# Optimization experiments

Hardware: AMD Instinct MI355X
Metric: run time of the kernel (lower is better)

## Reference

```python
import jax, jax.numpy as jnp
import numpy as np

M, K, N = 8192, 4096, 4096


def setup_inputs() -> dict:
    key = jax.random.key(0)
    k1, k2, k3 = jax.random.split(key, 3)
    inp = jax.random.normal(k1, (M, K), dtype=jnp.float32)
    weight = jax.random.normal(k2, (N, K), dtype=jnp.float32)
    bias = jax.random.normal(k3, (N,), dtype=jnp.bfloat16)
    return {"inp": inp, "weight": weight, "bias": bias}


def reference(inp, weight, bias):
    # FP8TensorMeta scales are all ones in the source module.
    scale = jnp.float32(1.0)       # quantization scale
    scale_inv = jnp.float32(1.0)   # dequantization scale (per operand)

    # cast_to_fp8: scale then saturate-cast to e4m3
    inp_fp8 = (inp * scale).astype(jnp.float8_e4m3fn)
    weight_fp8 = (weight * scale).astype(jnp.float8_e4m3fn)

    # fp8_gemm: dequantized GEMM with fp32 accumulation, bf16 bias, fp32 out
    out = jnp.einsum(
        "mk,nk->mn",
        inp_fp8.astype(jnp.float32),
        weight_fp8.astype(jnp.float32),
    ) * (scale_inv * scale_inv)
    out = out + bias.astype(jnp.float32)[None, :]
    return out
```

## Files before the change

kernel.cpp:

```cpp
#include <hip/hip_runtime.h>
#include <hip/hip_bf16.h>
#include <stdint.h>


#define MD 8192
#define KD 4096
#define ND 4096
#define BM 128
#define BN 128
#define BK 64

using f32x4  = __attribute__((ext_vector_type(4))) float;
using f32x16 = __attribute__((ext_vector_type(16))) float;
using i32x4  = __attribute__((ext_vector_type(4))) int;
using i32x8  = __attribute__((ext_vector_type(8))) int;

__global__ __launch_bounds__(256) void quant_fp8_fused_kernel(
    const float* __restrict__ inA, const float* __restrict__ inW,
    uint8_t* __restrict__ outA, uint8_t* __restrict__ outW) {
  const int NA4 = MD * KD / 4;
  const int NW4 = ND * KD / 4;
  const int tid = blockIdx.x * blockDim.x + threadIdx.x;
  const int stride = gridDim.x * blockDim.x;

  for (int i = tid; i < NA4; i += stride) {
    float4 f = ((const float4*)inA)[i];
    int v = 0;
    v = __builtin_amdgcn_cvt_pk_fp8_f32(f.x, f.y, v, false);
    v = __builtin_amdgcn_cvt_pk_fp8_f32(f.z, f.w, v, true);
    ((int*)outA)[i] = v;
  }
  for (int i = tid; i < NW4; i += stride) {
    float4 f = ((const float4*)inW)[i];
    int v = 0;
    v = __builtin_amdgcn_cvt_pk_fp8_f32(f.x, f.y, v, false);
    v = __builtin_amdgcn_cvt_pk_fp8_f32(f.z, f.w, v, true);
    ((int*)outW)[i] = v;
  }
}

__device__ __forceinline__ void gload16(const uint8_t* g, uint8_t* l) {
  __builtin_amdgcn_global_load_lds(
      (const __attribute__((address_space(1))) void*)g,
      (__attribute__((address_space(3))) void*)l, 16, 0, 0);
}

__global__ __launch_bounds__(256, 2) void fp8mx_gemm_bias_kernel(
    const uint8_t* __restrict__ A, const uint8_t* __restrict__ B,
    const __hip_bfloat16* __restrict__ bias, float* __restrict__ C) {
  __shared__ uint8_t sm[2][2][BM * BK];

  const int bid = blockIdx.x;
  const int chunk = bid & 7;
  const int local = bid >> 3;
  const int g = local >> 4, li = local & 15;
  const int tm = chunk * 8 + (g >> 3) * 4 + (li >> 2);
  const int tn = (g & 7) * 4 + (li & 3);

  const int t = threadIdx.x;
  const int w = t >> 6;
  const int l = t & 63;
  const int wm = w >> 1, wn = w & 1;
  const int r31 = l & 31, kh = l >> 5;

  const int row_a = t >> 2;
  const int gsw = (t & 3) ^ ((row_a >> 1) & 3);
  const size_t a0 = (size_t)(tm * BM + row_a) * KD + gsw * 16;
  const size_t a1 = a0 + (size_t)64 * KD;
  const size_t b0 = (size_t)(tn * BN + row_a) * KD + gsw * 16;
  const size_t b1 = b0 + (size_t)64 * KD;
  const int wd = w * 1024;

  const int s = (r31 >> 1) & 3;
  const int cLo = (((kh << 1) | 0) ^ s) * 16;
  const int cHi = (((kh << 1) | 1) ^ s) * 16;

  f32x16 acc[2][2];
#pragma unroll
  for (int fm = 0; fm < 2; ++fm)
#pragma unroll
    for (int fn = 0; fn < 2; ++fn)
#pragma unroll
      for (int r = 0; r < 16; ++r) acc[fm][fn][r] = 0.f;

  auto stage = [&](int buf, int kt) {
    const size_t ko = (size_t)kt * BK;
    gload16(A + a0 + ko, &sm[buf][0][wd]);
    gload16(A + a1 + ko, &sm[buf][0][4096 + wd]);
    gload16(B + b0 + ko, &sm[buf][1][wd]);
    gload16(B + b1 + ko, &sm[buf][1][4096 + wd]);
  };

  auto compute = [&](int buf) {
    const uint8_t* sa = &sm[buf][0][0];
    const uint8_t* sb = &sm[buf][1][0];
    i32x8 af[2], bf[2];
#pragma unroll
    for (int f = 0; f < 2; ++f) {
      const int ra = (wm * 64 + f * 32 + r31) * 64;
      i32x4 alo = *(const i32x4*)(sa + ra + cLo);
      i32x4 ahi = *(const i32x4*)(sa + ra + cHi);
      const int rb = (wn * 64 + f * 32 + r31) * 64;
      i32x4 blo = *(const i32x4*)(sb + rb + cLo);
      i32x4 bhi = *(const i32x4*)(sb + rb + cHi);
#pragma unroll
      for (int j = 0; j < 4; ++j) {
        af[f][j] = alo[j]; af[f][4 + j] = ahi[j];
        bf[f][j] = blo[j]; bf[f][4 + j] = bhi[j];
      }
    }
#pragma unroll
    for (int fm = 0; fm < 2; ++fm)
#pragma unroll
      for (int fn = 0; fn < 2; ++fn)
        acc[fm][fn] = __builtin_amdgcn_mfma_scale_f32_32x32x64_f8f6f4(
            af[fm], bf[fn], acc[fm][fn],
            0, 0,
            0, 0x7F7F7F7F,
            0, 0x7F7F7F7F);
  };

  const int NT = KD / BK;
  stage(0, 0);
  __syncthreads();
#pragma unroll 1
  for (int kt = 0; kt < NT - 1; ++kt) {
    const int cur = kt & 1;
    stage(cur ^ 1, kt + 1);
    compute(cur);
    __syncthreads();
  }
  compute((NT - 1) & 1);

#pragma unroll
  for (int fm = 0; fm < 2; ++fm)
#pragma unroll
    for (int fn = 0; fn < 2; ++fn) {
      const int col = tn * BN + wn * 64 + fn * 32 + r31;
      const float bv = __bfloat162float(bias[col]);
      const int row0 = tm * BM + wm * 64 + fm * 32 + 4 * kh;
      const f32x16 v = acc[fm][fn];
#pragma unroll
      for (int r = 0; r < 16; ++r) {
        const int row = row0 + (r & 3) + 8 * (r >> 2);
        C[(size_t)row * ND + col] = v[r] + bv;
      }
    }
}

extern "C" void kernel_launch(void* const* d_in, const int* in_sizes, int n_in,
                              void* d_out, int out_size, void* d_ws, size_t ws_size,
                              hipStream_t stream) {
  const float* inp = (const float*)d_in[0];
  const float* wgt = (const float*)d_in[1];
  const __hip_bfloat16* bias = (const __hip_bfloat16*)d_in[2];
  float* out = (float*)d_out;

  uint8_t* a8 = (uint8_t*)d_ws;
  uint8_t* b8 = a8 + (size_t)MD * KD;

  quant_fp8_fused_kernel<<<2048, 256, 0, stream>>>(inp, wgt, a8, b8);
  fp8mx_gemm_bias_kernel<<<2048, 256, 0, stream>>>(a8, b8, bias, out);
}
```

Before: 418.2 us.

## Enlarge GEMM tile to 256x128 and widen quantization stores to 16 bytes

The GEMM block tile grows from 128x128 to 256x128, so each wave computes a 128x64 sub-tile with eight 32x32 MFMA accumulators. This raises arithmetic intensity per LDS byte and halves the grid to 1024 blocks, and the block-to-tile swizzle is remapped for the new tile count. The quantization kernel now has each thread convert 16 floats and write one 16-byte store instead of 4-byte stores. The trade-offs are more accumulator registers, larger LDS use per block (possibly lowering occupancy), and fewer blocks to spread across CUs.

After: 399.7 us. 1.05x faster.

```diff
diff --git a/kernel.cpp b/kernel.cpp
--- a/kernel.cpp
+++ b/kernel.cpp
@@ -6,36 +6,38 @@
 #define MD 8192
 #define KD 4096
 #define ND 4096
-#define BM 128
+#define BM 256
 #define BN 128
 #define BK 64
 
-using f32x4  = __attribute__((ext_vector_type(4))) float;
 using f32x16 = __attribute__((ext_vector_type(16))) float;
 using i32x4  = __attribute__((ext_vector_type(4))) int;
 using i32x8  = __attribute__((ext_vector_type(8))) int;
 
+__device__ __forceinline__ int q4(float4 f) {
+  int v = 0;
+  v = __builtin_amdgcn_cvt_pk_fp8_f32(f.x, f.y, v, false);
+  v = __builtin_amdgcn_cvt_pk_fp8_f32(f.z, f.w, v, true);
+  return v;
+}
+
 __global__ __launch_bounds__(256) void quant_fp8_fused_kernel(
     const float* __restrict__ inA, const float* __restrict__ inW,
     uint8_t* __restrict__ outA, uint8_t* __restrict__ outW) {
-  const int NA4 = MD * KD / 4;
-  const int NW4 = ND * KD / 4;
+  const int NA16 = MD * KD / 16;
+  const int NW16 = ND * KD / 16;
   const int tid = blockIdx.x * blockDim.x + threadIdx.x;
   const int stride = gridDim.x * blockDim.x;
 
-  for (int i = tid; i < NA4; i += stride) {
-    float4 f = ((const float4*)inA)[i];
-    int v = 0;
-    v = __builtin_amdgcn_cvt_pk_fp8_f32(f.x, f.y, v, false);
-    v = __builtin_amdgcn_cvt_pk_fp8_f32(f.z, f.w, v, true);
-    ((int*)outA)[i] = v;
+  for (int i = tid; i < NA16; i += stride) {
+    const float4* p = (const float4*)inA + (size_t)i * 4;
+    int4 v = make_int4(q4(p[0]), q4(p[1]), q4(p[2]), q4(p[3]));
+    ((int4*)outA)[i] = v;
   }
-  for (int i = tid; i < NW4; i += stride) {
-    float4 f = ((const float4*)inW)[i];
-    int v = 0;
-    v = __builtin_amdgcn_cvt_pk_fp8_f32(f.x, f.y, v, false);
-    v = __builtin_amdgcn_cvt_pk_fp8_f32(f.z, f.w, v, true);
-    ((int*)outW)[i] = v;
+  for (int i = tid; i < NW16; i += stride) {
+    const float4* p = (const float4*)inW + (size_t)i * 4;
+    int4 v = make_int4(q4(p[0]), q4(p[1]), q4(p[2]), q4(p[3]));
+    ((int4*)outW)[i] = v;
   }
 }
 
@@ -48,14 +50,14 @@
 __global__ __launch_bounds__(256, 2) void fp8mx_gemm_bias_kernel(
     const uint8_t* __restrict__ A, const uint8_t* __restrict__ B,
     const __hip_bfloat16* __restrict__ bias, float* __restrict__ C) {
-  __shared__ uint8_t sm[2][2][BM * BK];
+  __shared__ uint8_t sm[2][24576];
 
   const int bid = blockIdx.x;
-  const int chunk = bid & 7;
+  const int xcd = bid & 7;
   const int local = bid >> 3;
-  const int g = local >> 4, li = local & 15;
-  const int tm = chunk * 8 + (g >> 3) * 4 + (li >> 2);
-  const int tn = (g & 7) * 4 + (li & 3);
+  const int grp = local >> 3, li = local & 7;
+  const int tm = xcd * 4 + (grp >> 3) * 2 + (li >> 2);
+  const int tn = (grp & 7) * 4 + (li & 3);
 
   const int t = threadIdx.x;
   const int w = t >> 6;
@@ -63,21 +65,19 @@
   const int wm = w >> 1, wn = w & 1;
   const int r31 = l & 31, kh = l >> 5;
 
-  const int row_a = t >> 2;
-  const int gsw = (t & 3) ^ ((row_a >> 1) & 3);
-  const size_t a0 = (size_t)(tm * BM + row_a) * KD + gsw * 16;
-  const size_t a1 = a0 + (size_t)64 * KD;
-  const size_t b0 = (size_t)(tn * BN + row_a) * KD + gsw * 16;
-  const size_t b1 = b0 + (size_t)64 * KD;
+  const int row_s = t >> 2;
+  const int gsw = (t & 3) ^ ((row_s >> 1) & 3);
+  const size_t abase = (size_t)(tm * BM + row_s) * KD + gsw * 16;
+  const size_t bbase = (size_t)(tn * BN + row_s) * KD + gsw * 16;
   const int wd = w * 1024;
 
   const int s = (r31 >> 1) & 3;
   const int cLo = (((kh << 1) | 0) ^ s) * 16;
   const int cHi = (((kh << 1) | 1) ^ s) * 16;
 
-  f32x16 acc[2][2];
+  f32x16 acc[4][2];
 #pragma unroll
-  for (int fm = 0; fm < 2; ++fm)
+  for (int fm = 0; fm < 4; ++fm)
 #pragma unroll
     for (int fn = 0; fn < 2; ++fn)
 #pragma unroll
@@ -85,32 +85,38 @@
 
   auto stage = [&](int buf, int kt) {
     const size_t ko = (size_t)kt * BK;
-    gload16(A + a0 + ko, &sm[buf][0][wd]);
-    gload16(A + a1 + ko, &sm[buf][0][4096 + wd]);
-    gload16(B + b0 + ko, &sm[buf][1][wd]);
-    gload16(B + b1 + ko, &sm[buf][1][4096 + wd]);
+    uint8_t* la = &sm[buf][wd];
+#pragma unroll
+    for (int rnd = 0; rnd < 4; ++rnd)
+      gload16(A + abase + (size_t)rnd * 64 * KD + ko, la + rnd * 4096);
+    uint8_t* lb = &sm[buf][16384 + wd];
+#pragma unroll
+    for (int rnd = 0; rnd < 2; ++rnd)
+      gload16(B + bbase + (size_t)rnd * 64 * KD + ko, lb + rnd * 4096);
   };
 
   auto compute = [&](int buf) {
-    const uint8_t* sa = &sm[buf][0][0];
-    const uint8_t* sb = &sm[buf][1][0];
-    i32x8 af[2], bf[2];
+    const uint8_t* sa = &sm[buf][0];
+    const uint8_t* sb = &sm[buf][16384];
+    i32x8 af[4], bf[2];
 #pragma unroll
-    for (int f = 0; f < 2; ++f) {
-      const int ra = (wm * 64 + f * 32 + r31) * 64;
-      i32x4 alo = *(const i32x4*)(sa + ra + cLo);
-      i32x4 ahi = *(const i32x4*)(sa + ra + cHi);
-      const int rb = (wn * 64 + f * 32 + r31) * 64;
-      i32x4 blo = *(const i32x4*)(sb + rb + cLo);
-      i32x4 bhi = *(const i32x4*)(sb + rb + cHi);
+    for (int fm = 0; fm < 4; ++fm) {
+      const int ra = (wm * 128 + fm * 32 + r31) * 64;
+      i32x4 lo = *(const i32x4*)(sa + ra + cLo);
+      i32x4 hi = *(const i32x4*)(sa + ra + cHi);
 #pragma unroll
-      for (int j = 0; j < 4; ++j) {
-        af[f][j] = alo[j]; af[f][4 + j] = ahi[j];
-        bf[f][j] = blo[j]; bf[f][4 + j] = bhi[j];
-      }
+      for (int j = 0; j < 4; ++j) { af[fm][j] = lo[j]; af[fm][4 + j] = hi[j]; }
     }
 #pragma unroll
-    for (int fm = 0; fm < 2; ++fm)
+    for (int fn = 0; fn < 2; ++fn) {
+      const int rb = (wn * 64 + fn * 32 + r31) * 64;
+      i32x4 lo = *(const i32x4*)(sb + rb + cLo);
+      i32x4 hi = *(const i32x4*)(sb + rb + cHi);
+#pragma unroll
+      for (int j = 0; j < 4; ++j) { bf[fn][j] = lo[j]; bf[fn][4 + j] = hi[j]; }
+    }
+#pragma unroll
+    for (int fm = 0; fm < 4; ++fm)
 #pragma unroll
       for (int fn = 0; fn < 2; ++fn)
         acc[fm][fn] = __builtin_amdgcn_mfma_scale_f32_32x32x64_f8f6f4(
@@ -133,12 +139,12 @@
   compute((NT - 1) & 1);
 
 #pragma unroll
-  for (int fm = 0; fm < 2; ++fm)
+  for (int fn = 0; fn < 2; ++fn) {
+    const int col = tn * BN + wn * 64 + fn * 32 + r31;
+    const float bv = __bfloat162float(bias[col]);
 #pragma unroll
-    for (int fn = 0; fn < 2; ++fn) {
-      const int col = tn * BN + wn * 64 + fn * 32 + r31;
-      const float bv = __bfloat162float(bias[col]);
-      const int row0 = tm * BM + wm * 64 + fm * 32 + 4 * kh;
+    for (int fm = 0; fm < 4; ++fm) {
+      const int row0 = tm * BM + wm * 128 + fm * 32 + 4 * kh;
       const f32x16 v = acc[fm][fn];
 #pragma unroll
       for (int r = 0; r < 16; ++r) {
@@ -146,6 +152,7 @@
         C[(size_t)row * ND + col] = v[r] + bv;
       }
     }
+  }
 }
 
 extern "C" void kernel_launch(void* const* d_in, const int* in_sizes, int n_in,
@@ -160,5 +167,5 @@
   uint8_t* b8 = a8 + (size_t)MD * KD;
 
   quant_fp8_fused_kernel<<<2048, 256, 0, stream>>>(inp, wgt, a8, b8);
-  fp8mx_gemm_bias_kernel<<<2048, 256, 0, stream>>>(a8, b8, bias, out);
+  fp8mx_gemm_bias_kernel<<<1024, 256, 0, stream>>>(a8, b8, bias, out);
 }
```
